# Kernel optimization log

Hardware: AMD Instinct MI355X
Metric: run time of the kernel (lower is better)

## Reference

```python
import jax, jax.numpy as jnp
import numpy as np

DIM = 512
NUM_EXPERTS = 16
HIDDEN = 512
OUT_DIM = DIM // 4  # 128


def setup_inputs() -> dict:
    key = jax.random.key(0)
    k_x, k_w1, k_w2 = jax.random.split(key, 3)
    x = jax.random.normal(k_x, (4, 2048, DIM), dtype=jnp.float32)
    # init_(t): uniform(-1/sqrt(last_dim), 1/sqrt(last_dim))
    s1 = 1.0 / np.sqrt(HIDDEN)
    s2 = 1.0 / np.sqrt(OUT_DIM)
    w1 = jax.random.uniform(k_w1, (NUM_EXPERTS, DIM, HIDDEN), dtype=jnp.float32, minval=-s1, maxval=s1)
    w2 = jax.random.uniform(k_w2, (NUM_EXPERTS, HIDDEN, OUT_DIM), dtype=jnp.float32, minval=-s2, maxval=s2)
    return {"x": x, "w1": w1, "w2": w2}


def reference(x, w1, w2):
    # x: [b, n, d]; w1: [e, d, h]; w2: [e, h, d4]
    hidden = jnp.einsum("bnd,edh->benh", x, w1)          # [b, e, n, h]
    hidden = jax.nn.gelu(hidden, approximate=False)       # exact GELU = torch nn.GELU default
    out = jnp.einsum("benh,ehd->bnde", hidden, w2)        # [b, n, d4, e]
    return out
```

## Files before the change

### kernel.cpp

```cpp
#include <hip/hip_runtime.h>
#include <stdint.h>

typedef short bf16x8 __attribute__((ext_vector_type(8)));
typedef float f32x4 __attribute__((ext_vector_type(4)));

__device__ __forceinline__ void async_cp16(const void* g, short* lds) {
  __builtin_amdgcn_global_load_lds(
      (const __attribute__((address_space(1))) void*)g,
      (__attribute__((address_space(3))) void*)lds, 16, 0, 0);
}

__device__ __forceinline__ float gelu_f(float v) {
  float z = 1.5957691216057308f * (v + 0.044715f * v * v * v);
  return __fdividef(v, 1.0f + __expf(-z));
}

__device__ __forceinline__ short f2bf(float x) {
  uint32_t u = __float_as_uint(x);
  u += 0x7fffu + ((u >> 16) & 1u);
  return (short)(u >> 16);
}

__global__ __launch_bounds__(256)
void prep_all(const float* __restrict__ x, const float* __restrict__ w1,
              const float* __restrict__ w2, short* __restrict__ Xb,
              short* __restrict__ w1t, short* __restrict__ w2t)
{
  __shared__ __align__(16) short T[64][72];
  const int b = blockIdx.x;
  const int t = threadIdx.x;

  if (b < 2048) {
    const int idx = (b * 256 + t) * 8;
    bf16x8 o;
#pragma unroll
    for (int u = 0; u < 8; ++u) o[u] = f2bf(x[idx + u]);
    *(bf16x8*)(Xb + idx) = o;
    return;
  }

  const float* src; short* dst; int e, r0, c0, R, C;
  if (b < 3072) {
    int idx = b - 2048; e = idx >> 6; int rem = idx & 63;
    r0 = (rem >> 3) * 64; c0 = (rem & 7) * 64; R = 512; C = 512;
    src = w1; dst = w1t;
  } else {
    int idx = b - 3072; e = idx >> 4; int rem = idx & 15;
    r0 = (rem >> 1) * 64; c0 = (rem & 1) * 64; R = 512; C = 128;
    src = w2; dst = w2t;
  }
  const float* s = src + (size_t)e * R * C;
  short* d       = dst + (size_t)e * R * C;
  const int i = t >> 3, j8 = t & 7;
#pragma unroll
  for (int p = 0; p < 2; ++p) {
    int ii = i + p * 32;
#pragma unroll
    for (int u = 0; u < 8; ++u)
      T[ii][j8 * 8 + u] = f2bf(s[(size_t)(r0 + ii) * C + c0 + j8 * 8 + u]);
  }
  __syncthreads();
#pragma unroll
  for (int p = 0; p < 2; ++p) {
    int ii = i + p * 32;
    bf16x8 v;
#pragma unroll
    for (int u = 0; u < 8; ++u) v[u] = T[j8 * 8 + u][ii];
    *(bf16x8*)(d + (size_t)(c0 + ii) * R + r0 + j8 * 8) = v;
  }
}

__global__ __launch_bounds__(256, 2)
void moe_kernel(const short* __restrict__ Xb, const short* __restrict__ W1T,
                const short* __restrict__ W2T, void* __restrict__ O, int staged)
{
  __shared__ __align__(16) short SM[25600];
  short* const Ws0 = SM;
  short* const Ws1 = SM + 4096;
  short* const Xs0 = SM + 8192;
  short* const Xs1 = SM + 12288;
  short* const HL  = SM + 8192;

  const int tid = threadIdx.x;
  const int l = tid & 63, w = tid >> 6;
  const int wm = w & 1, wn = w >> 1;
  const int e    = blockIdx.x >> 6;
  const int tile = blockIdx.x & 63;

  const int lrow = l >> 2, lq = l & 3;
  int ldso[2];
  const char *xg[2], *w1g[2], *w2g[2];
#pragma unroll
  for (int c = 0; c < 2; ++c) {
    int prow = w * 32 + c * 16 + lrow;
    int qg = lq ^ ((prow >> 1) & 3);
    ldso[c] = (w * 32 + c * 16) * 32;
    xg[c]  = (const char*)Xb  + (size_t)(tile * 128 + prow) * 1024 + qg * 16;
    w1g[c] = (const char*)W1T + (size_t)e * 524288 + (size_t)prow * 1024 + qg * 16;
    w2g[c] = (const char*)W2T + (size_t)e * 131072 + (size_t)prow * 1024 + qg * 16;
  }

  const int lm = l & 15;
  const int slot = (l >> 4) ^ ((lm >> 1) & 3);
  const int aoff = (wm * 64 + lm) * 32 + slot * 8;
  const int boff = (wn * 64 + lm) * 32 + slot * 8;
  const int hro  = (wm * 64 + lm) * 136 + (l >> 4) * 8;
  const int hwo  = (wm * 64 + (l >> 4) * 4) * 136 + wn * 64 + lm;

  f32x4 acc2[4][4];
#pragma unroll
  for (int i = 0; i < 4; ++i)
#pragma unroll
    for (int j = 0; j < 4; ++j) acc2[i][j] = (f32x4){0.f, 0.f, 0.f, 0.f};

#pragma unroll
  for (int c = 0; c < 2; ++c) {
    async_cp16(xg[c],  Xs0 + ldso[c]);
    async_cp16(w1g[c], Ws0 + ldso[c]);
  }

  for (int hc = 0; hc < 4; ++hc) {
    f32x4 acc1[4][4];
#pragma unroll
    for (int i = 0; i < 4; ++i)
#pragma unroll
      for (int j = 0; j < 4; ++j) acc1[i][j] = (f32x4){0.f, 0.f, 0.f, 0.f};

    const size_t w1hc = (size_t)hc * 131072;

#pragma unroll
    for (int kk = 0; kk < 16; ++kk) {
      __syncthreads();
      if (kk < 15) {
        short* xb = ((kk + 1) & 1) ? Xs1 : Xs0;
        short* wb = ((kk + 1) & 1) ? Ws1 : Ws0;
#pragma unroll
        for (int c = 0; c < 2; ++c) {
          async_cp16(xg[c] + (kk + 1) * 64,         xb + ldso[c]);
          async_cp16(w1g[c] + w1hc + (kk + 1) * 64, wb + ldso[c]);
        }
      } else {
#pragma unroll
        for (int c = 0; c < 2; ++c)
          async_cp16(w2g[c] + hc * 256, Ws0 + ldso[c]);
      }
      const short* xb = (kk & 1) ? Xs1 : Xs0;
      const short* wb = (kk & 1) ? Ws1 : Ws0;
      bf16x8 af[4], bfr[4];
#pragma unroll
      for (int t = 0; t < 4; ++t) af[t]  = *(const bf16x8*)(xb + aoff + t * 512);
#pragma unroll
      for (int t = 0; t < 4; ++t) bfr[t] = *(const bf16x8*)(wb + boff + t * 512);
#pragma unroll
      for (int i = 0; i < 4; ++i)
#pragma unroll
        for (int j = 0; j < 4; ++j)
          acc1[i][j] = __builtin_amdgcn_mfma_f32_16x16x32_bf16(af[i], bfr[j], acc1[i][j], 0, 0, 0);
    }

    __syncthreads();

#pragma unroll
    for (int i = 0; i < 4; ++i)
#pragma unroll
      for (int j = 0; j < 4; ++j)
#pragma unroll
        for (int r = 0; r < 4; ++r)
          HL[hwo + i * 2176 + r * 136 + j * 16] = f2bf(gelu_f(acc1[i][j][r]));

#pragma unroll
    for (int s = 0; s < 4; ++s) {
      __syncthreads();
      if (s < 3) {
        short* wb = ((s + 1) & 1) ? Ws1 : Ws0;
#pragma unroll
        for (int c = 0; c < 2; ++c)
          async_cp16(w2g[c] + hc * 256 + (s + 1) * 64, wb + ldso[c]);
      }
      const short* wb = (s & 1) ? Ws1 : Ws0;
      bf16x8 af[4], bfr[4];
#pragma unroll
      for (int t = 0; t < 4; ++t) af[t]  = *(const bf16x8*)(HL + hro + t * 2176 + s * 32);
#pragma unroll
      for (int t = 0; t < 4; ++t) bfr[t] = *(const bf16x8*)(wb + boff + t * 512);
#pragma unroll
      for (int i = 0; i < 4; ++i)
#pragma unroll
        for (int j = 0; j < 4; ++j)
          acc2[i][j] = __builtin_amdgcn_mfma_f32_16x16x32_bf16(af[i], bfr[j], acc2[i][j], 0, 0, 0);
    }

    if (hc < 3) {
      __syncthreads();
#pragma unroll
      for (int c = 0; c < 2; ++c) {
        async_cp16(xg[c],                              Xs0 + ldso[c]);
        async_cp16(w1g[c] + (size_t)(hc + 1) * 131072, Ws0 + ldso[c]);
      }
    }
  }

  const int d4 = wn * 64 + lm;
  const int lqr = (l >> 4) * 4;
  if (staged) {
    unsigned short* Ob = (unsigned short*)O;
    const size_t base = ((size_t)e * 8192 + tile * 128 + wm * 64 + lqr) * 128 + d4;
#pragma unroll
    for (int i = 0; i < 4; ++i)
#pragma unroll
      for (int r = 0; r < 4; ++r)
#pragma unroll
        for (int j = 0; j < 4; ++j)
          Ob[base + (size_t)(i * 16 + r) * 128 + j * 16] = (unsigned short)f2bf(acc2[i][j][r]);
  } else {
    float* Of = (float*)O;
    const size_t rowb = (size_t)tile * 128 + wm * 64 + lqr;
    const size_t base = (rowb * 128 + d4) * 16 + e;
#pragma unroll
    for (int i = 0; i < 4; ++i)
#pragma unroll
      for (int r = 0; r < 4; ++r)
#pragma unroll
        for (int j = 0; j < 4; ++j)
          Of[base + (size_t)(i * 16 + r) * 2048 + j * 256] = acc2[i][j][r];
  }
}

__global__ __launch_bounds__(256, 2)
void permute_kernel(const unsigned short* __restrict__ OUTs, float* __restrict__ OUT)
{
  __shared__ float T[8 * 16 * 132];
  const int t = threadIdx.x;
  const int r0 = blockIdx.x * 8;
#pragma unroll
  for (int it = 0; it < 8; ++it) {
    int v = it * 256 + t;
    int e = v >> 7, rem = v & 127, r = rem >> 4, q8 = rem & 15;
    bf16x8 d = *(const bf16x8*)(OUTs + ((size_t)e * 8192 + r0 + r) * 128 + q8 * 8);
#pragma unroll
    for (int u = 0; u < 8; ++u)
      T[(r * 16 + e) * 132 + q8 * 8 + u] =
          __uint_as_float(((uint32_t)(unsigned short)d[u]) << 16);
  }
  __syncthreads();
#pragma unroll
  for (int it = 0; it < 16; ++it) {
    int u = it * 256 + t;
    int r = u >> 9;
    int c4 = (u & 511) * 4;
    int d4 = c4 >> 4, e0 = c4 & 15;
    f32x4 o;
#pragma unroll
    for (int i = 0; i < 4; ++i) o[i] = T[(r * 16 + e0 + i) * 132 + d4];
    *(f32x4*)(OUT + (size_t)(r0 + r) * 2048 + c4) = o;
  }
}

extern "C" void kernel_launch(void* const* d_in, const int* in_sizes, int n_in,
                              void* d_out, int out_size, void* d_ws, size_t ws_size,
                              hipStream_t stream)
{
  const float* x  = (const float*)d_in[0];
  const float* w1 = (const float*)d_in[1];
  const float* w2 = (const float*)d_in[2];
  float* out = (float*)d_out;

  short* Xb  = (short*)d_ws;
  short* w1t = Xb + 4194304;
  short* w2t = w1t + 4194304;
  unsigned short* OUTs = (unsigned short*)((char*)d_ws + 18874368);
  const bool staged = ws_size >= 52428800ULL;

  prep_all<<<dim3(3328), 256, 0, stream>>>(x, w1, w2, Xb, w1t, w2t);
  moe_kernel<<<dim3(1024), 256, 0, stream>>>(Xb, w1t, w2t,
                                             staged ? (void*)OUTs : (void*)out,
                                             staged ? 1 : 0);
  if (staged)
    permute_kernel<<<dim3(1024), 256, 0, stream>>>(OUTs, out);
}
```

Before: 224.4 us.

## Prefetch W2 slices early and load half directly to registers, cutting barriers

The second GEMM stage previously streamed four W2 k-slices through LDS with a barrier per slice. Now the second slice is prefetched into LDS before the GELU epilogue, and the last two slices are loaded straight from global memory into registers, leaving one barrier per hidden chunk. The prep kernel also stages fp32 values in a padded float tile with vector loads and converts to bf16 on the transposed read. The aim is fewer syncs and more overlap of W2 loads with GELU work, at the cost of extra VGPR pressure under launch bounds of 256 threads with two blocks per SM, plus uncoalesced global reads for the register path.

```diff
diff --git a/kernel.cpp b/kernel.cpp
--- a/kernel.cpp
+++ b/kernel.cpp
@@ -26,7 +26,7 @@
               const float* __restrict__ w2, short* __restrict__ Xb,
               short* __restrict__ w1t, short* __restrict__ w2t)
 {
-  __shared__ __align__(16) short T[64][72];
+  __shared__ float TF[64 * 65];
   const int b = blockIdx.x;
   const int t = threadIdx.x;
 
@@ -55,9 +55,12 @@
 #pragma unroll
   for (int p = 0; p < 2; ++p) {
     int ii = i + p * 32;
-#pragma unroll
-    for (int u = 0; u < 8; ++u)
-      T[ii][j8 * 8 + u] = f2bf(s[(size_t)(r0 + ii) * C + c0 + j8 * 8 + u]);
+    const float* rp = s + (size_t)(r0 + ii) * C + c0 + j8 * 8;
+    f32x4 a = *(const f32x4*)rp;
+    f32x4 bb = *(const f32x4*)(rp + 4);
+    float* Tp = &TF[ii * 65 + j8 * 8];
+#pragma unroll
+    for (int u = 0; u < 4; ++u) { Tp[u] = a[u]; Tp[4 + u] = bb[u]; }
   }
   __syncthreads();
 #pragma unroll
@@ -65,7 +68,7 @@
     int ii = i + p * 32;
     bf16x8 v;
 #pragma unroll
-    for (int u = 0; u < 8; ++u) v[u] = T[j8 * 8 + u][ii];
+    for (int u = 0; u < 8; ++u) v[u] = f2bf(TF[(j8 * 8 + u) * 65 + ii]);
     *(bf16x8*)(d + (size_t)(c0 + ii) * R + r0 + j8 * 8) = v;
   }
 }
@@ -106,6 +109,7 @@
   const int boff = (wn * 64 + lm) * 32 + slot * 8;
   const int hro  = (wm * 64 + lm) * 136 + (l >> 4) * 8;
   const int hwo  = (wm * 64 + (l >> 4) * 4) * 136 + wn * 64 + lm;
+  const short* w2row = W2T + (size_t)e * 65536 + (size_t)(wn * 64 + lm) * 512 + (l >> 4) * 8;
 
   f32x4 acc2[4][4];
 #pragma unroll
@@ -161,6 +165,10 @@
     __syncthreads();
 
 #pragma unroll
+    for (int c = 0; c < 2; ++c)
+      async_cp16(w2g[c] + hc * 256 + 64, Ws1 + ldso[c]);
+
+#pragma unroll
     for (int i = 0; i < 4; ++i)
 #pragma unroll
       for (int j = 0; j < 4; ++j)
@@ -168,26 +176,41 @@
         for (int r = 0; r < 4; ++r)
           HL[hwo + i * 2176 + r * 136 + j * 16] = f2bf(gelu_f(acc1[i][j][r]));
 
-#pragma unroll
-    for (int s = 0; s < 4; ++s) {
-      __syncthreads();
-      if (s < 3) {
-        short* wb = ((s + 1) & 1) ? Ws1 : Ws0;
-#pragma unroll
-        for (int c = 0; c < 2; ++c)
-          async_cp16(w2g[c] + hc * 256 + (s + 1) * 64, wb + ldso[c]);
+    __syncthreads();
+
+    {
+      bf16x8 bg[2][4];
+#pragma unroll
+      for (int u = 0; u < 2; ++u)
+#pragma unroll
+        for (int t = 0; t < 4; ++t)
+          bg[u][t] = *(const bf16x8*)(w2row + (size_t)t * 8192 + hc * 128 + 64 + u * 32);
+
+#pragma unroll
+      for (int u = 0; u < 2; ++u) {
+        const short* wb = u ? Ws1 : Ws0;
+        bf16x8 af[4], bfr[4];
+#pragma unroll
+        for (int t = 0; t < 4; ++t) af[t]  = *(const bf16x8*)(HL + hro + t * 2176 + u * 32);
+#pragma unroll
+        for (int t = 0; t < 4; ++t) bfr[t] = *(const bf16x8*)(wb + boff + t * 512);
+#pragma unroll
+        for (int i = 0; i < 4; ++i)
+#pragma unroll
+          for (int j = 0; j < 4; ++j)
+            acc2[i][j] = __builtin_amdgcn_mfma_f32_16x16x32_bf16(af[i], bfr[j], acc2[i][j], 0, 0, 0);
       }
-      const short* wb = (s & 1) ? Ws1 : Ws0;
-      bf16x8 af[4], bfr[4];
-#pragma unroll
-      for (int t = 0; t < 4; ++t) af[t]  = *(const bf16x8*)(HL + hro + t * 2176 + s * 32);
-#pragma unroll
-      for (int t = 0; t < 4; ++t) bfr[t] = *(const bf16x8*)(wb + boff + t * 512);
-#pragma unroll
-      for (int i = 0; i < 4; ++i)
-#pragma unroll
-        for (int j = 0; j < 4; ++j)
-          acc2[i][j] = __builtin_amdgcn_mfma_f32_16x16x32_bf16(af[i], bfr[j], acc2[i][j], 0, 0, 0);
+#pragma unroll
+      for (int u = 0; u < 2; ++u) {
+        bf16x8 af[4];
+#pragma unroll
+        for (int t = 0; t < 4; ++t) af[t] = *(const bf16x8*)(HL + hro + t * 2176 + 64 + u * 32);
+#pragma unroll
+        for (int i = 0; i < 4; ++i)
+#pragma unroll
+          for (int j = 0; j < 4; ++j)
+            acc2[i][j] = __builtin_amdgcn_mfma_f32_16x16x32_bf16(af[i], bg[u][j], acc2[i][j], 0, 0, 0);
+      }
     }
 
     if (hc < 3) {
```

After: 236.1 us. 1.05x slower.
